# Optimization experiments

Hardware: AMD Instinct MI355X
Metric: run time of the kernel (lower is better)

The kernel has to match this reference:

```python
import jax, jax.numpy as jnp
import numpy as np

N = 100000
E = 3200000
IN_DIM = 256
HID = 64
OUT = 40


def setup_inputs() -> dict:
    key = jax.random.key(0)
    ks = jax.random.split(key, 8)
    x = jax.random.normal(ks[0], (N, IN_DIM), dtype=jnp.float32)
    edge_index = jax.random.randint(ks[1], (2, E), 0, N, dtype=jnp.int64)
    # Glorot-ish init for weights
    W1 = jax.random.normal(ks[2], (IN_DIM, HID), dtype=jnp.float32) / np.sqrt(IN_DIM)
    b1 = jnp.zeros((HID,), dtype=jnp.float32)
    W2 = jax.random.normal(ks[3], (HID, HID), dtype=jnp.float32) / np.sqrt(HID)
    b2 = jnp.zeros((HID,), dtype=jnp.float32)
    W3 = jax.random.normal(ks[4], (HID, OUT), dtype=jnp.float32) / np.sqrt(HID)
    b3 = jax.random.normal(ks[5], (OUT,), dtype=jnp.float32) * 0.01
    return {"x": x, "edge_index": edge_index,
            "W1": W1, "b1": b1, "W2": W2, "b2": b2, "W3": W3, "b3": b3}


def _gcn_norm(edge_index, n):
    # Add self-loops, compute symmetric normalization deg^-1/2 A deg^-1/2
    loop = jnp.arange(n, dtype=edge_index.dtype)
    src = jnp.concatenate([edge_index[0], loop])
    dst = jnp.concatenate([edge_index[1], loop])
    deg = jax.ops.segment_sum(jnp.ones_like(dst, dtype=jnp.float32), dst,
                              num_segments=n)
    dinv = jnp.where(deg > 0, jax.lax.rsqrt(deg), 0.0)
    norm = dinv[src] * dinv[dst]  # [E+N]
    return src, dst, norm


def _gcn_conv(x, src, dst, norm, W, b, n):
    h = x @ W                                  # transform first (small dim)
    msg = h[src] * norm[:, None]               # gather + scale
    out = jax.ops.segment_sum(msg, dst, num_segments=n)  # scatter-add
    return out + b


def reference(x, edge_index, W1, b1, W2, b2, W3, b3):
    n = x.shape[0]
    src, dst, norm = _gcn_norm(edge_index, n)
    h = jax.nn.relu(_gcn_conv(x, src, dst, norm, W1, b1, n))
    h = jax.nn.relu(_gcn_conv(h, src, dst, norm, W2, b2, n))
    logits = h @ W3 + b3
    return jax.nn.log_softmax(logits, axis=1)
```

## Files before the change

kernel.cpp:

```cpp
#include <hip/hip_runtime.h>
#include <hip/hip_fp16.h>
#include <cstdint>


constexpr int CHUNK = 8192;
constexpr int BKCAP = 8192;

__global__ __launch_bounds__(256) void p2_localsort(
        const int* __restrict__ esrc, const int* __restrict__ edst, int E,
        unsigned* __restrict__ pairs1, int* __restrict__ cntMat,
        int* __restrict__ startMat, int NBK) {
    __shared__ int hist[1024];
    __shared__ int wsum[256];
    __shared__ unsigned lp[CHUNK];
    const int t = threadIdx.x, blk = blockIdx.x;
    const int base = blk * CHUNK;
    const int cnt = min(CHUNK, E - base);
    for (int i = t; i < 1024; i += 256) hist[i] = 0;
    __syncthreads();
    for (int i = t; i < cnt; i += 256) atomicAdd(&hist[edst[base + i] >> 7], 1);
    __syncthreads();
    int h0 = hist[4*t], h1 = hist[4*t+1], h2 = hist[4*t+2], h3 = hist[4*t+3];
    int s = h0 + h1 + h2 + h3;
    wsum[t] = s; __syncthreads();
    #pragma unroll
    for (int o = 1; o < 256; o <<= 1) {
        int x = (t >= o) ? wsum[t - o] : 0;
        __syncthreads(); wsum[t] += x; __syncthreads();
    }
    int run = wsum[t] - s;
    int e0 = run, e1 = run + h0, e2 = e1 + h1, e3 = e2 + h2;
    hist[4*t] = e0; hist[4*t+1] = e1; hist[4*t+2] = e2; hist[4*t+3] = e3;
    if (4*t     < NBK) { cntMat[(size_t)blk*NBK + 4*t]     = h0; startMat[(size_t)blk*NBK + 4*t]     = e0; }
    if (4*t + 1 < NBK) { cntMat[(size_t)blk*NBK + 4*t + 1] = h1; startMat[(size_t)blk*NBK + 4*t + 1] = e1; }
    if (4*t + 2 < NBK) { cntMat[(size_t)blk*NBK + 4*t + 2] = h2; startMat[(size_t)blk*NBK + 4*t + 2] = e2; }
    if (4*t + 3 < NBK) { cntMat[(size_t)blk*NBK + 4*t + 3] = h3; startMat[(size_t)blk*NBK + 4*t + 3] = e3; }
    __syncthreads();
    for (int i = t; i < cnt; i += 256) {
        int d = edst[base + i];
        int pos = atomicAdd(&hist[d >> 7], 1);
        lp[pos] = ((unsigned)(d & 127) << 17) | (unsigned)esrc[base + i];
    }
    __syncthreads();
    for (int i = t; i < cnt; i += 256) pairs1[base + i] = lp[i];
}

__global__ __launch_bounds__(256) void p3_colscan(int* __restrict__ cntMat,
        int* __restrict__ TB, int nchunks, int NBK) {
    __shared__ int buf[512];
    const int t = threadIdx.x, b = blockIdx.x;
    int v0 = (t < nchunks) ? cntMat[(size_t)t*NBK + b] : 0;
    int v1 = (t + 256 < nchunks) ? cntMat[(size_t)(t + 256)*NBK + b] : 0;
    buf[t] = v0; buf[t + 256] = v1; __syncthreads();
    #pragma unroll
    for (int o = 1; o < 512; o <<= 1) {
        int x0 = (t >= o) ? buf[t - o] : 0;
        int x1 = (t + 256 >= o) ? buf[t + 256 - o] : 0;
        __syncthreads(); buf[t] += x0; buf[t + 256] += x1; __syncthreads();
    }
    if (t < nchunks) cntMat[(size_t)t*NBK + b] = buf[t] - v0;
    if (t + 256 < nchunks) cntMat[(size_t)(t + 256)*NBK + b] = buf[t + 256] - v1;
    if (t == 0) TB[b] = buf[511];
}

__global__ __launch_bounds__(256) void p4_scan(const int* __restrict__ TB,
        int* __restrict__ bucketBase, int NBK, int E) {
    __shared__ int buf[1024];
    __shared__ int wsum[256];
    const int t = threadIdx.x;
    for (int i = t; i < 1024; i += 256) buf[i] = (i < NBK) ? TB[i] : 0;
    __syncthreads();
    int h0 = buf[4*t], h1 = buf[4*t+1], h2 = buf[4*t+2], h3 = buf[4*t+3];
    int s = h0 + h1 + h2 + h3;
    wsum[t] = s; __syncthreads();
    #pragma unroll
    for (int o = 1; o < 256; o <<= 1) {
        int x = (t >= o) ? wsum[t - o] : 0;
        __syncthreads(); wsum[t] += x; __syncthreads();
    }
    int run = wsum[t] - s;
    int e0 = run, e1 = run + h0, e2 = e1 + h1, e3 = e2 + h2;
    if (4*t     < NBK) bucketBase[4*t]     = e0;
    if (4*t + 1 < NBK) bucketBase[4*t + 1] = e1;
    if (4*t + 2 < NBK) bucketBase[4*t + 2] = e2;
    if (4*t + 3 < NBK) bucketBase[4*t + 3] = e3;
    if (t == 0) bucketBase[NBK] = E;
}

__global__ __launch_bounds__(256) void p6_sortcsr(
        const unsigned* __restrict__ pairs1, const int* __restrict__ cumMat,
        const int* __restrict__ startMat, const int* __restrict__ TB,
        const int* __restrict__ bucketBase, int nchunks, int NBK,
        int* __restrict__ csrc, int* __restrict__ rofs,
        float* __restrict__ dinv, int N, int E) {
    __shared__ unsigned lp[BKCAP];
    __shared__ int ccum[512];
    __shared__ int cstart[512];
    __shared__ int hist[128];
    __shared__ int sc[128];
    __shared__ int foffs[128];
    const int t = threadIdx.x, b = blockIdx.x;
    const int total0 = TB[b];
    const int total = min(total0, BKCAP);
    const int base = bucketBase[b];
    for (int i = t; i < nchunks; i += 256) {
        ccum[i]   = cumMat[(size_t)i * NBK + b];
        cstart[i] = startMat[(size_t)i * NBK + b];
    }
    if (t < 128) hist[t] = 0;
    if (t == 0) ccum[nchunks] = total0;
    __syncthreads();
    for (int i = t; i < total; i += 256) {
        int lo = 0, hi = nchunks - 1;
        while (lo < hi) {
            int mid = (lo + hi + 1) >> 1;
            if (ccum[mid] <= i) lo = mid; else hi = mid - 1;
        }
        unsigned v = pairs1[(size_t)lo * CHUNK + cstart[lo] + (i - ccum[lo])];
        lp[i] = v;
        atomicAdd(&hist[v >> 17], 1);
    }
    __syncthreads();
    if (t < 128) sc[t] = hist[t];
    __syncthreads();
    #pragma unroll
    for (int o = 1; o < 128; o <<= 1) {
        int x = (t >= o && t < 128) ? sc[t - o] : 0;
        __syncthreads();
        if (t < 128) sc[t] += x;
        __syncthreads();
    }
    if (t < 128) {
        int excl = sc[t] - hist[t];
        foffs[t] = excl;
        int node = b * 128 + t;
        if (node < N) {
            rofs[node] = base + excl;
            dinv[node] = rsqrtf((float)hist[t] + 1.0f);
        }
    }
    if (b == 0 && t == 255) rofs[N] = E;
    __syncthreads();
    for (int i = t; i < total; i += 256) {
        unsigned v = lp[i];
        int pos = atomicAdd(&foffs[v >> 17], 1);
        csrc[base + pos] = (int)(v & 0x1FFFFu);
    }
}

template<int K>
__global__ __launch_bounds__(256) void k_gemm(const float* __restrict__ X,
        const float* __restrict__ Wm, const float* __restrict__ dinv,
        __half* __restrict__ G, int nrows) {
    constexpr int BK = 32;
    constexpr int NCH = K / BK;
    constexpr int XP = 68;
    __shared__ float Xs[BK * XP];
    __shared__ float Ws[BK * 64];
    const int t = threadIdx.x;
    const int cg = t & 15;
    const int rg = t >> 4;
    const int brow = blockIdx.x * 64;

    float acc[4][4];
    #pragma unroll
    for (int r = 0; r < 4; ++r)
        #pragma unroll
        for (int c = 0; c < 4; ++c) acc[r][c] = 0.f;

    for (int ch = 0; ch < NCH; ++ch) {
        if (ch) __syncthreads();
        #pragma unroll
        for (int i = 0; i < 2; ++i) {
            int f = t + i * 256;
            int r = f >> 3, c4 = f & 7;
            int gr = brow + r;
            float4 v = make_float4(0.f, 0.f, 0.f, 0.f);
            if (gr < nrows)
                v = *(const float4*)(X + (size_t)gr * K + ch * BK + c4 * 4);
            int rsw = r ^ (c4 << 2);
            Xs[(c4 * 4 + 0) * XP + rsw] = v.x;
            Xs[(c4 * 4 + 1) * XP + rsw] = v.y;
            Xs[(c4 * 4 + 2) * XP + rsw] = v.z;
            Xs[(c4 * 4 + 3) * XP + rsw] = v.w;
        }
        #pragma unroll
        for (int i = 0; i < 2; ++i) {
            int f = t + i * 256;
            int k = f >> 4, c4 = f & 15;
            *(float4*)(Ws + k * 64 + c4 * 4) =
                *(const float4*)(Wm + (size_t)(ch * BK + k) * 64 + c4 * 4);
        }
        __syncthreads();

        #pragma unroll
        for (int k = 0; k < BK; ++k) {
            const int xsw = (k >> 2) << 2;
            float4 xa = *(const float4*)(Xs + k * XP + ((rg * 4) ^ xsw));
            float4 wv = *(const float4*)(Ws + k * 64 + cg * 4);
            acc[0][0] += xa.x * wv.x; acc[0][1] += xa.x * wv.y;
            acc[0][2] += xa.x * wv.z; acc[0][3] += xa.x * wv.w;
            acc[1][0] += xa.y * wv.x; acc[1][1] += xa.y * wv.y;
            acc[1][2] += xa.y * wv.z; acc[1][3] += xa.y * wv.w;
            acc[2][0] += xa.z * wv.x; acc[2][1] += xa.z * wv.y;
            acc[2][2] += xa.z * wv.z; acc[2][3] += xa.z * wv.w;
            acc[3][0] += xa.w * wv.x; acc[3][1] += xa.w * wv.y;
            acc[3][2] += xa.w * wv.z; acc[3][3] += xa.w * wv.w;
        }
    }
    #pragma unroll
    for (int r = 0; r < 4; ++r) {
        int gr = brow + rg * 4 + r;
        if (gr < nrows) {
            float dv = dinv[gr];
            __half2 h01 = __floats2half2_rn(acc[r][0] * dv, acc[r][1] * dv);
            __half2 h23 = __floats2half2_rn(acc[r][2] * dv, acc[r][3] * dv);
            uint2 pk;
            pk.x = *(unsigned*)&h01; pk.y = *(unsigned*)&h23;
            *(uint2*)(G + (size_t)gr * 64 + cg * 4) = pk;
        }
    }
}

#define ACC8(A0, A1, V) { \
    float2 f0_ = __half22float2(*(const __half2*)&(V).x); \
    float2 f1_ = __half22float2(*(const __half2*)&(V).y); \
    float2 f2_ = __half22float2(*(const __half2*)&(V).z); \
    float2 f3_ = __half22float2(*(const __half2*)&(V).w); \
    (A0).x += f0_.x; (A0).y += f0_.y; (A0).z += f1_.x; (A0).w += f1_.y; \
    (A1).x += f2_.x; (A1).y += f2_.y; (A1).z += f3_.x; (A1).w += f3_.y; }

__global__ __launch_bounds__(256) void k_agg(const __half* __restrict__ G,
        const int* __restrict__ rofs, const int* __restrict__ csrc,
        const float* __restrict__ dinv, const float* __restrict__ bias,
        float* __restrict__ H, int nrows) {
    const int l = threadIdx.x & 63;
    const int g = l >> 3;
    const int p = l & 7;
    const int d = blockIdx.x * 4 + (threadIdx.x >> 6);
    if (d >= nrows) return;
    const int beg = rofs[d], end = rofs[d + 1];
    float4 a0 = make_float4(0.f, 0.f, 0.f, 0.f);
    float4 a1 = make_float4(0.f, 0.f, 0.f, 0.f);

    int e = beg + g;
    for (; e + 8 < end; e += 16) {
        int s0 = csrc[e];
        int s1 = csrc[e + 8];
        uint4 v0 = *(const uint4*)(G + (size_t)s0 * 64 + p * 8);
        uint4 v1 = *(const uint4*)(G + (size_t)s1 * 64 + p * 8);
        ACC8(a0, a1, v0)
        ACC8(a0, a1, v1)
    }
    if (e < end) {
        int s = csrc[e];
        uint4 v = *(const uint4*)(G + (size_t)s * 64 + p * 8);
        ACC8(a0, a1, v)
    }
    #pragma unroll
    for (int off = 8; off <= 32; off <<= 1) {
        a0.x += __shfl_xor(a0.x, off); a0.y += __shfl_xor(a0.y, off);
        a0.z += __shfl_xor(a0.z, off); a0.w += __shfl_xor(a0.w, off);
        a1.x += __shfl_xor(a1.x, off); a1.y += __shfl_xor(a1.y, off);
        a1.z += __shfl_xor(a1.z, off); a1.w += __shfl_xor(a1.w, off);
    }
    if (g == 0) {
        uint4 sv = *(const uint4*)(G + (size_t)d * 64 + p * 8);
        float2 s0 = __half22float2(*(const __half2*)&sv.x);
        float2 s1 = __half22float2(*(const __half2*)&sv.y);
        float2 s2 = __half22float2(*(const __half2*)&sv.z);
        float2 s3 = __half22float2(*(const __half2*)&sv.w);
        const float dv = dinv[d];
        const float4* B4 = (const float4*)bias;
        float4 b0 = B4[p * 2], b1 = B4[p * 2 + 1];
        float4 o0, o1;
        o0.x = fmaxf((a0.x + s0.x) * dv + b0.x, 0.f);
        o0.y = fmaxf((a0.y + s0.y) * dv + b0.y, 0.f);
        o0.z = fmaxf((a0.z + s1.x) * dv + b0.z, 0.f);
        o0.w = fmaxf((a0.w + s1.y) * dv + b0.w, 0.f);
        o1.x = fmaxf((a1.x + s2.x) * dv + b1.x, 0.f);
        o1.y = fmaxf((a1.y + s2.y) * dv + b1.y, 0.f);
        o1.z = fmaxf((a1.z + s3.x) * dv + b1.z, 0.f);
        o1.w = fmaxf((a1.w + s3.y) * dv + b1.w, 0.f);
        float4* H4 = (float4*)(H + (size_t)d * 64 + p * 8);
        H4[0] = o0; H4[1] = o1;
    }
}

__global__ __launch_bounds__(256) void k_final(const float* __restrict__ H,
        const float* __restrict__ W3, const float* __restrict__ b3,
        float* __restrict__ out, int nrows) {
    constexpr int HP = 68;
    constexpr int OP = 44;
    __shared__ float wl[64 * 40];
    __shared__ float bl[40];
    __shared__ float Hs[256 * HP];
    const int t = threadIdx.x;
    for (int i = t; i < 640; i += 256)
        ((float4*)wl)[i] = ((const float4*)W3)[i];
    if (t < 40) bl[t] = b3[t];
    const int brow = blockIdx.x * 256;
    const int rows = min(256, nrows - brow);
    for (int i = t; i < rows * 16; i += 256) {
        int r = i >> 4, c = i & 15;
        float4 v = ((const float4*)(H + (size_t)(brow + r) * 64))[c];
        *(float4*)&Hs[r * HP + c * 4] = v;
    }
    __syncthreads();

    float acc[40];
    float lse = 0.f;
    if (t < rows) {
        #pragma unroll
        for (int j = 0; j < 40; ++j) acc[j] = bl[j];
        #pragma unroll
        for (int k4 = 0; k4 < 16; ++k4) {
            float4 h4 = *(const float4*)&Hs[t * HP + k4 * 4];
            float hv[4] = {h4.x, h4.y, h4.z, h4.w};
            #pragma unroll
            for (int c = 0; c < 4; ++c) {
                const float4* wr = (const float4*)(wl + (k4 * 4 + c) * 40);
                #pragma unroll
                for (int j4 = 0; j4 < 10; ++j4) {
                    float4 wv = wr[j4];
                    acc[j4 * 4 + 0] += hv[c] * wv.x;
                    acc[j4 * 4 + 1] += hv[c] * wv.y;
                    acc[j4 * 4 + 2] += hv[c] * wv.z;
                    acc[j4 * 4 + 3] += hv[c] * wv.w;
                }
            }
        }
        float m = acc[0];
        #pragma unroll
        for (int j = 1; j < 40; ++j) m = fmaxf(m, acc[j]);
        float s = 0.f;
        #pragma unroll
        for (int j = 0; j < 40; ++j) s += expf(acc[j] - m);
        lse = m + logf(s);
    }
    __syncthreads();
    float* Os = Hs;
    if (t < rows) {
        #pragma unroll
        for (int j4 = 0; j4 < 10; ++j4)
            *(float4*)&Os[t * OP + j4 * 4] =
                make_float4(acc[j4 * 4 + 0] - lse, acc[j4 * 4 + 1] - lse,
                            acc[j4 * 4 + 2] - lse, acc[j4 * 4 + 3] - lse);
    }
    __syncthreads();
    for (int i = t; i < rows * 40; i += 256) {
        int r = i / 40, c = i - r * 40;
        out[(size_t)brow * 40 + i] = Os[r * OP + c];
    }
}

extern "C" void kernel_launch(void* const* d_in, const int* in_sizes, int n_in,
                              void* d_out, int out_size, void* d_ws, size_t ws_size,
                              hipStream_t stream) {
    const float* x  = (const float*)d_in[0];
    const int*   ei = (const int*)d_in[1];
    const float* W1 = (const float*)d_in[2];
    const float* b1 = (const float*)d_in[3];
    const float* W2 = (const float*)d_in[4];
    const float* b2 = (const float*)d_in[5];
    const float* W3 = (const float*)d_in[6];
    const float* b3 = (const float*)d_in[7];
    float* out = (float*)d_out;

    const int HID = in_sizes[3];
    const int IND = in_sizes[2] / HID;
    const int N   = in_sizes[0] / IND;
    const int E   = in_sizes[1] / 2;
    (void)HID; (void)n_in; (void)out_size; (void)ws_size;

    const int NBK     = (N + 127) >> 7;
    const int nchunks = (E + CHUNK - 1) / CHUNK;

    char* ws = (char*)d_ws;
    size_t off = 0;
    auto alloc = [&](size_t bytes) -> char* {
        char* p = ws + off;
        off = (off + bytes + 255) & ~(size_t)255;
        return p;
    };
    size_t gbytes = (size_t)N * 64 * 2;
    size_t p1bytes = (size_t)E * 4;
    int*      cntMat     = (int*)     alloc((size_t)nchunks * NBK * 4);
    int*      startMat   = (int*)     alloc((size_t)nchunks * NBK * 4);
    int*      TB         = (int*)     alloc((size_t)NBK * 4);
    int*      bucketBase = (int*)     alloc(((size_t)NBK + 1) * 4);
    float*    dinv       = (float*)   alloc((size_t)N * 4);
    int*      rofs       = (int*)     alloc(((size_t)N + 1) * 4);
    int*      csrc       = (int*)     alloc((size_t)E * 4);
    __half*   g          = (__half*)  alloc(gbytes > p1bytes ? gbytes : p1bytes);
    float*    h          = (float*)   alloc((size_t)N * 64 * 4);
    unsigned* pairs1     = (unsigned*)g;

    const int* esrc = ei;
    const int* edst = ei + E;
    const int gM = (N + 63) / 64;
    const int gN = (N + 255) / 256;

    p2_localsort<<<nchunks, 256, 0, stream>>>(esrc, edst, E, pairs1, cntMat, startMat, NBK);
    p3_colscan  <<<NBK, 256, 0, stream>>>(cntMat, TB, nchunks, NBK);
    p4_scan     <<<1, 256, 0, stream>>>(TB, bucketBase, NBK, E);
    p6_sortcsr  <<<NBK, 256, 0, stream>>>(pairs1, cntMat, startMat, TB, bucketBase,
                                          nchunks, NBK, csrc, rofs, dinv, N, E);

    k_gemm<256> <<<gM, 256, 0, stream>>>(x, W1, dinv, g, N);
    k_agg       <<<(N + 3) / 4, 256, 0, stream>>>(g, rofs, csrc, dinv, b1, h, N);
    k_gemm<64>  <<<gM, 256, 0, stream>>>(h, W2, dinv, g, N);
    k_agg       <<<(N + 3) / 4, 256, 0, stream>>>(g, rofs, csrc, dinv, b2, h, N);
    k_final     <<<gN, 256, 0, stream>>>(h, W3, b3, out, N);
}
```

Measured before the change: 289.5 us.

## Use bf16 MFMA for feature GEMMs and half-precision accumulation in aggregation

Replaces the fp32 SIMT register-tiled GEMM with a persistent-wave kernel that converts X and W to bf16 and uses 16x16x32 MFMA instructions, with W staged transposed in LDS. Separately, the neighbour aggregation now accumulates in packed fp16 (hadd2) and reduces via shuffles of packed halves instead of fp32. This aims to cut GEMM ALU time and aggregation instruction count, at the cost of reduced precision (bf16 inputs, fp16 accumulation over ~33 neighbours) and scalar 2-byte output stores. The tiling also assumes nrows is a multiple of 16, which holds for N=100000.

```diff
diff --git a/kernel.cpp b/kernel.cpp
--- a/kernel.cpp
+++ b/kernel.cpp
@@ -5,6 +5,15 @@
 
 constexpr int CHUNK = 8192;
 constexpr int BKCAP = 8192;
+
+typedef __attribute__((ext_vector_type(8))) short bf16x8;
+typedef __attribute__((ext_vector_type(4))) float f32x4;
+
+__device__ __forceinline__ int cvt2bf(float a, float b) {
+    int r;
+    asm volatile("v_cvt_pk_bf16_f32 %0, %1, %2" : "=v"(r) : "v"(a), "v"(b));
+    return r;
+}
 
 __global__ __launch_bounds__(256) void p2_localsort(
         const int* __restrict__ esrc, const int* __restrict__ edst, int E,
@@ -152,83 +161,55 @@
 __global__ __launch_bounds__(256) void k_gemm(const float* __restrict__ X,
         const float* __restrict__ Wm, const float* __restrict__ dinv,
         __half* __restrict__ G, int nrows) {
-    constexpr int BK = 32;
-    constexpr int NCH = K / BK;
-    constexpr int XP = 68;
-    __shared__ float Xs[BK * XP];
-    __shared__ float Ws[BK * 64];
+    constexpr int KP = K + 8;
+    __shared__ unsigned short Wt[64 * KP];
     const int t = threadIdx.x;
-    const int cg = t & 15;
-    const int rg = t >> 4;
-    const int brow = blockIdx.x * 64;
-
-    float acc[4][4];
-    #pragma unroll
-    for (int r = 0; r < 4; ++r)
-        #pragma unroll
-        for (int c = 0; c < 4; ++c) acc[r][c] = 0.f;
-
-    for (int ch = 0; ch < NCH; ++ch) {
-        if (ch) __syncthreads();
-        #pragma unroll
-        for (int i = 0; i < 2; ++i) {
-            int f = t + i * 256;
-            int r = f >> 3, c4 = f & 7;
-            int gr = brow + r;
-            float4 v = make_float4(0.f, 0.f, 0.f, 0.f);
-            if (gr < nrows)
-                v = *(const float4*)(X + (size_t)gr * K + ch * BK + c4 * 4);
-            int rsw = r ^ (c4 << 2);
-            Xs[(c4 * 4 + 0) * XP + rsw] = v.x;
-            Xs[(c4 * 4 + 1) * XP + rsw] = v.y;
-            Xs[(c4 * 4 + 2) * XP + rsw] = v.z;
-            Xs[(c4 * 4 + 3) * XP + rsw] = v.w;
-        }
-        #pragma unroll
-        for (int i = 0; i < 2; ++i) {
-            int f = t + i * 256;
-            int k = f >> 4, c4 = f & 15;
-            *(float4*)(Ws + k * 64 + c4 * 4) =
-                *(const float4*)(Wm + (size_t)(ch * BK + k) * 64 + c4 * 4);
-        }
-        __syncthreads();
-
-        #pragma unroll
-        for (int k = 0; k < BK; ++k) {
-            const int xsw = (k >> 2) << 2;
-            float4 xa = *(const float4*)(Xs + k * XP + ((rg * 4) ^ xsw));
-            float4 wv = *(const float4*)(Ws + k * 64 + cg * 4);
-            acc[0][0] += xa.x * wv.x; acc[0][1] += xa.x * wv.y;
-            acc[0][2] += xa.x * wv.z; acc[0][3] += xa.x * wv.w;
-            acc[1][0] += xa.y * wv.x; acc[1][1] += xa.y * wv.y;
-            acc[1][2] += xa.y * wv.z; acc[1][3] += xa.y * wv.w;
-            acc[2][0] += xa.z * wv.x; acc[2][1] += xa.z * wv.y;
-            acc[2][2] += xa.z * wv.z; acc[2][3] += xa.z * wv.w;
-            acc[3][0] += xa.w * wv.x; acc[3][1] += xa.w * wv.y;
-            acc[3][2] += xa.w * wv.z; acc[3][3] += xa.w * wv.w;
-        }
-    }
-    #pragma unroll
-    for (int r = 0; r < 4; ++r) {
-        int gr = brow + rg * 4 + r;
-        if (gr < nrows) {
-            float dv = dinv[gr];
-            __half2 h01 = __floats2half2_rn(acc[r][0] * dv, acc[r][1] * dv);
-            __half2 h23 = __floats2half2_rn(acc[r][2] * dv, acc[r][3] * dv);
-            uint2 pk;
-            pk.x = *(unsigned*)&h01; pk.y = *(unsigned*)&h23;
-            *(uint2*)(G + (size_t)gr * 64 + cg * 4) = pk;
-        }
-    }
-}
-
-#define ACC8(A0, A1, V) { \
-    float2 f0_ = __half22float2(*(const __half2*)&(V).x); \
-    float2 f1_ = __half22float2(*(const __half2*)&(V).y); \
-    float2 f2_ = __half22float2(*(const __half2*)&(V).z); \
-    float2 f3_ = __half22float2(*(const __half2*)&(V).w); \
-    (A0).x += f0_.x; (A0).y += f0_.y; (A0).z += f1_.x; (A0).w += f1_.y; \
-    (A1).x += f2_.x; (A1).y += f2_.y; (A1).z += f3_.x; (A1).w += f3_.y; }
+    for (int i = t; i < K * 64; i += 256) {
+        int k = i >> 6, n = i & 63;
+        Wt[n * KP + k] = (unsigned short)(cvt2bf(Wm[i], Wm[i]) & 0xFFFF);
+    }
+    __syncthreads();
+    const int l  = t & 63;
+    const int c16 = l & 15;
+    const int g4  = l >> 4;
+    const int wglob  = blockIdx.x * 4 + (t >> 6);
+    const int nwaves = gridDim.x * 4;
+    const int ntiles = nrows >> 4;
+
+    for (int tile = wglob; tile < ntiles; tile += nwaves) {
+        const int rbase = tile * 16;
+        f32x4 acc[4] = {{0,0,0,0},{0,0,0,0},{0,0,0,0},{0,0,0,0}};
+        const float* xrow = X + (size_t)(rbase + c16) * K + g4 * 8;
+        #pragma unroll
+        for (int kc = 0; kc < K / 32; ++kc) {
+            float4 u = *(const float4*)(xrow + kc * 32);
+            float4 v = *(const float4*)(xrow + kc * 32 + 4);
+            int4 ap;
+            ap.x = cvt2bf(u.x, u.y); ap.y = cvt2bf(u.z, u.w);
+            ap.z = cvt2bf(v.x, v.y); ap.w = cvt2bf(v.z, v.w);
+            bf16x8 a = *(bf16x8*)&ap;
+            #pragma unroll
+            for (int cg = 0; cg < 4; ++cg) {
+                bf16x8 bb = *(bf16x8*)(&Wt[(cg * 16 + c16) * KP + kc * 32 + g4 * 8]);
+                acc[cg] = __builtin_amdgcn_mfma_f32_16x16x32_bf16(a, bb, acc[cg], 0, 0, 0);
+            }
+        }
+        #pragma unroll
+        for (int r = 0; r < 4; ++r) {
+            int grow = rbase + g4 * 4 + r;
+            float dv = dinv[grow];
+            #pragma unroll
+            for (int cg = 0; cg < 4; ++cg)
+                G[(size_t)grow * 64 + cg * 16 + c16] = __float2half(acc[cg][r] * dv);
+        }
+    }
+}
+
+#define ACC8H(HA, V) { \
+    HA[0] = __hadd2(HA[0], *(const __half2*)&(V).x); \
+    HA[1] = __hadd2(HA[1], *(const __half2*)&(V).y); \
+    HA[2] = __hadd2(HA[2], *(const __half2*)&(V).z); \
+    HA[3] = __hadd2(HA[3], *(const __half2*)&(V).w); }
 
 __global__ __launch_bounds__(256) void k_agg(const __half* __restrict__ G,
         const int* __restrict__ rofs, const int* __restrict__ csrc,
@@ -240,8 +221,9 @@
     const int d = blockIdx.x * 4 + (threadIdx.x >> 6);
     if (d >= nrows) return;
     const int beg = rofs[d], end = rofs[d + 1];
-    float4 a0 = make_float4(0.f, 0.f, 0.f, 0.f);
-    float4 a1 = make_float4(0.f, 0.f, 0.f, 0.f);
+    __half2 ha[4];
+    #pragma unroll
+    for (int q = 0; q < 4; ++q) ha[q] = __half2(__float2half(0.f), __float2half(0.f));
 
     int e = beg + g;
     for (; e + 8 < end; e += 16) {
@@ -249,22 +231,25 @@
         int s1 = csrc[e + 8];
         uint4 v0 = *(const uint4*)(G + (size_t)s0 * 64 + p * 8);
         uint4 v1 = *(const uint4*)(G + (size_t)s1 * 64 + p * 8);
-        ACC8(a0, a1, v0)
-        ACC8(a0, a1, v1)
+        ACC8H(ha, v0)
+        ACC8H(ha, v1)
     }
     if (e < end) {
         int s = csrc[e];
         uint4 v = *(const uint4*)(G + (size_t)s * 64 + p * 8);
-        ACC8(a0, a1, v)
+        ACC8H(ha, v)
     }
     #pragma unroll
     for (int off = 8; off <= 32; off <<= 1) {
-        a0.x += __shfl_xor(a0.x, off); a0.y += __shfl_xor(a0.y, off);
-        a0.z += __shfl_xor(a0.z, off); a0.w += __shfl_xor(a0.w, off);
-        a1.x += __shfl_xor(a1.x, off); a1.y += __shfl_xor(a1.y, off);
-        a1.z += __shfl_xor(a1.z, off); a1.w += __shfl_xor(a1.w, off);
+        #pragma unroll
+        for (int q = 0; q < 4; ++q) {
+            int o = __shfl_xor(*(int*)&ha[q], off);
+            ha[q] = __hadd2(ha[q], *(__half2*)&o);
+        }
     }
     if (g == 0) {
+        float2 a0 = __half22float2(ha[0]), a1 = __half22float2(ha[1]);
+        float2 a2 = __half22float2(ha[2]), a3 = __half22float2(ha[3]);
         uint4 sv = *(const uint4*)(G + (size_t)d * 64 + p * 8);
         float2 s0 = __half22float2(*(const __half2*)&sv.x);
         float2 s1 = __half22float2(*(const __half2*)&sv.y);
@@ -276,12 +261,12 @@
         float4 o0, o1;
         o0.x = fmaxf((a0.x + s0.x) * dv + b0.x, 0.f);
         o0.y = fmaxf((a0.y + s0.y) * dv + b0.y, 0.f);
-        o0.z = fmaxf((a0.z + s1.x) * dv + b0.z, 0.f);
-        o0.w = fmaxf((a0.w + s1.y) * dv + b0.w, 0.f);
-        o1.x = fmaxf((a1.x + s2.x) * dv + b1.x, 0.f);
-        o1.y = fmaxf((a1.y + s2.y) * dv + b1.y, 0.f);
-        o1.z = fmaxf((a1.z + s3.x) * dv + b1.z, 0.f);
-        o1.w = fmaxf((a1.w + s3.y) * dv + b1.w, 0.f);
+        o0.z = fmaxf((a1.x + s1.x) * dv + b0.z, 0.f);
+        o0.w = fmaxf((a1.y + s1.y) * dv + b0.w, 0.f);
+        o1.x = fmaxf((a2.x + s2.x) * dv + b1.x, 0.f);
+        o1.y = fmaxf((a2.y + s2.y) * dv + b1.y, 0.f);
+        o1.z = fmaxf((a3.x + s3.x) * dv + b1.z, 0.f);
+        o1.w = fmaxf((a3.y + s3.y) * dv + b1.w, 0.f);
         float4* H4 = (float4*)(H + (size_t)d * 64 + p * 8);
         H4[0] = o0; H4[1] = o1;
     }
@@ -398,7 +383,7 @@
 
     const int* esrc = ei;
     const int* edst = ei + E;
-    const int gM = (N + 63) / 64;
+    const int gG = 782;
     const int gN = (N + 255) / 256;
 
     p2_localsort<<<nchunks, 256, 0, stream>>>(esrc, edst, E, pairs1, cntMat, startMat, NBK);
@@ -407,9 +392,9 @@
     p6_sortcsr  <<<NBK, 256, 0, stream>>>(pairs1, cntMat, startMat, TB, bucketBase,
                                           nchunks, NBK, csrc, rofs, dinv, N, E);
 
-    k_gemm<256> <<<gM, 256, 0, stream>>>(x, W1, dinv, g, N);
+    k_gemm<256> <<<gG, 256, 0, stream>>>(x, W1, dinv, g, N);
     k_agg       <<<(N + 3) / 4, 256, 0, stream>>>(g, rofs, csrc, dinv, b1, h, N);
-    k_gemm<64>  <<<gM, 256, 0, stream>>>(h, W2, dinv, g, N);
+    k_gemm<64>  <<<gG, 256, 0, stream>>>(h, W2, dinv, g, N);
     k_agg       <<<(N + 3) / 4, 256, 0, stream>>>(g, rofs, csrc, dinv, b2, h, N);
     k_final     <<<gN, 256, 0, stream>>>(h, W3, b3, out, N);
 }
```

New measurement: 270.2 us. -6.7%, faster.

## Fuse W2 GEMM into first aggregation and final projection into second

Applied to the files above, without the earlier changes.

The second-layer GEMM moves into the first aggregation kernel and the W3 projection plus log-softmax into the second, using wavefront shuffles over the per-node hidden vector. This removes the fp32 H round trip and two kernel launches. Gather accumulation also switches from fp32 to packed half2 adds, which cuts ALU work but can lose precision on high-degree nodes. Each aggregation block now loads the weight matrix into shared memory and runs a 64-step shuffle-FMA loop per node, which is extra per-block overhead.

```diff
diff --git a/kernel.cpp b/kernel.cpp
--- a/kernel.cpp
+++ b/kernel.cpp
@@ -222,136 +222,145 @@
     }
 }
 
-#define ACC8(A0, A1, V) { \
-    float2 f0_ = __half22float2(*(const __half2*)&(V).x); \
-    float2 f1_ = __half22float2(*(const __half2*)&(V).y); \
-    float2 f2_ = __half22float2(*(const __half2*)&(V).z); \
-    float2 f3_ = __half22float2(*(const __half2*)&(V).w); \
-    (A0).x += f0_.x; (A0).y += f0_.y; (A0).z += f1_.x; (A0).w += f1_.y; \
-    (A1).x += f2_.x; (A1).y += f2_.y; (A1).z += f3_.x; (A1).w += f3_.y; }
-
-__global__ __launch_bounds__(256) void k_agg(const __half* __restrict__ G,
+#define ACC8H(HA, V) { \
+    HA[0] = __hadd2(HA[0], *(const __half2*)&(V).x); \
+    HA[1] = __hadd2(HA[1], *(const __half2*)&(V).y); \
+    HA[2] = __hadd2(HA[2], *(const __half2*)&(V).z); \
+    HA[3] = __hadd2(HA[3], *(const __half2*)&(V).w); }
+
+#define GATHER_REDUCE(G_, beg_, end_, g_, p_, HA) { \
+    int e = (beg_) + (g_); \
+    for (; e + 8 < (end_); e += 16) { \
+        int s0 = csrc[e]; \
+        int s1 = csrc[e + 8]; \
+        uint4 v0 = *(const uint4*)((G_) + (size_t)s0 * 64 + (p_) * 8); \
+        uint4 v1 = *(const uint4*)((G_) + (size_t)s1 * 64 + (p_) * 8); \
+        ACC8H(HA, v0) \
+        ACC8H(HA, v1) \
+    } \
+    if (e < (end_)) { \
+        int s = csrc[e]; \
+        uint4 v = *(const uint4*)((G_) + (size_t)s * 64 + (p_) * 8); \
+        ACC8H(HA, v) \
+    } \
+    _Pragma("unroll") \
+    for (int off = 8; off <= 32; off <<= 1) { \
+        _Pragma("unroll") \
+        for (int q = 0; q < 4; ++q) { \
+            int o = __shfl_xor(*(int*)&HA[q], off); \
+            HA[q] = __hadd2(HA[q], *(__half2*)&o); \
+        } \
+    } }
+
+__global__ __launch_bounds__(256) void k_agg_mid(const __half* __restrict__ G,
         const int* __restrict__ rofs, const int* __restrict__ csrc,
-        const float* __restrict__ dinv, const float* __restrict__ bias,
-        float* __restrict__ H, int nrows) {
-    const int l = threadIdx.x & 63;
+        const float* __restrict__ dinv, const float* __restrict__ b1,
+        const float* __restrict__ W2, __half* __restrict__ G2, int nrows) {
+    __shared__ float W2s[64 * 64];
+    const int t = threadIdx.x;
+    for (int i = t; i < 1024; i += 256)
+        ((float4*)W2s)[i] = ((const float4*)W2)[i];
+    __syncthreads();
+    const int l = t & 63;
     const int g = l >> 3;
     const int p = l & 7;
-    const int d = blockIdx.x * 4 + (threadIdx.x >> 6);
+    const int d = blockIdx.x * 4 + (t >> 6);
     if (d >= nrows) return;
     const int beg = rofs[d], end = rofs[d + 1];
-    float4 a0 = make_float4(0.f, 0.f, 0.f, 0.f);
-    float4 a1 = make_float4(0.f, 0.f, 0.f, 0.f);
-
-    int e = beg + g;
-    for (; e + 8 < end; e += 16) {
-        int s0 = csrc[e];
-        int s1 = csrc[e + 8];
-        uint4 v0 = *(const uint4*)(G + (size_t)s0 * 64 + p * 8);
-        uint4 v1 = *(const uint4*)(G + (size_t)s1 * 64 + p * 8);
-        ACC8(a0, a1, v0)
-        ACC8(a0, a1, v1)
-    }
-    if (e < end) {
-        int s = csrc[e];
-        uint4 v = *(const uint4*)(G + (size_t)s * 64 + p * 8);
-        ACC8(a0, a1, v)
-    }
-    #pragma unroll
-    for (int off = 8; off <= 32; off <<= 1) {
-        a0.x += __shfl_xor(a0.x, off); a0.y += __shfl_xor(a0.y, off);
-        a0.z += __shfl_xor(a0.z, off); a0.w += __shfl_xor(a0.w, off);
-        a1.x += __shfl_xor(a1.x, off); a1.y += __shfl_xor(a1.y, off);
-        a1.z += __shfl_xor(a1.z, off); a1.w += __shfl_xor(a1.w, off);
-    }
-    if (g == 0) {
-        uint4 sv = *(const uint4*)(G + (size_t)d * 64 + p * 8);
-        float2 s0 = __half22float2(*(const __half2*)&sv.x);
-        float2 s1 = __half22float2(*(const __half2*)&sv.y);
-        float2 s2 = __half22float2(*(const __half2*)&sv.z);
-        float2 s3 = __half22float2(*(const __half2*)&sv.w);
-        const float dv = dinv[d];
-        const float4* B4 = (const float4*)bias;
-        float4 b0 = B4[p * 2], b1 = B4[p * 2 + 1];
-        float4 o0, o1;
-        o0.x = fmaxf((a0.x + s0.x) * dv + b0.x, 0.f);
-        o0.y = fmaxf((a0.y + s0.y) * dv + b0.y, 0.f);
-        o0.z = fmaxf((a0.z + s1.x) * dv + b0.z, 0.f);
-        o0.w = fmaxf((a0.w + s1.y) * dv + b0.w, 0.f);
-        o1.x = fmaxf((a1.x + s2.x) * dv + b1.x, 0.f);
-        o1.y = fmaxf((a1.y + s2.y) * dv + b1.y, 0.f);
-        o1.z = fmaxf((a1.z + s3.x) * dv + b1.z, 0.f);
-        o1.w = fmaxf((a1.w + s3.y) * dv + b1.w, 0.f);
-        float4* H4 = (float4*)(H + (size_t)d * 64 + p * 8);
-        H4[0] = o0; H4[1] = o1;
-    }
-}
-
-__global__ __launch_bounds__(256) void k_final(const float* __restrict__ H,
+    __half2 ha[4];
+    #pragma unroll
+    for (int q = 0; q < 4; ++q) ha[q] = __half2(__float2half(0.f), __float2half(0.f));
+    GATHER_REDUCE(G, beg, end, g, p, ha)
+
+    uint4 sv = *(const uint4*)(G + (size_t)d * 64 + p * 8);
+    const float dv = dinv[d];
+    float4 bb0 = *(const float4*)(b1 + p * 8);
+    float4 bb1 = *(const float4*)(b1 + p * 8 + 4);
+    float2 a0 = __half22float2(ha[0]), a1 = __half22float2(ha[1]);
+    float2 a2 = __half22float2(ha[2]), a3 = __half22float2(ha[3]);
+    float2 s0 = __half22float2(*(const __half2*)&sv.x);
+    float2 s1 = __half22float2(*(const __half2*)&sv.y);
+    float2 s2 = __half22float2(*(const __half2*)&sv.z);
+    float2 s3 = __half22float2(*(const __half2*)&sv.w);
+    float h1[8];
+    h1[0] = fmaxf((a0.x + s0.x) * dv + bb0.x, 0.f);
+    h1[1] = fmaxf((a0.y + s0.y) * dv + bb0.y, 0.f);
+    h1[2] = fmaxf((a1.x + s1.x) * dv + bb0.z, 0.f);
+    h1[3] = fmaxf((a1.y + s1.y) * dv + bb0.w, 0.f);
+    h1[4] = fmaxf((a2.x + s2.x) * dv + bb1.x, 0.f);
+    h1[5] = fmaxf((a2.y + s2.y) * dv + bb1.y, 0.f);
+    h1[6] = fmaxf((a3.x + s3.x) * dv + bb1.z, 0.f);
+    h1[7] = fmaxf((a3.y + s3.y) * dv + bb1.w, 0.f);
+
+    float acc = 0.f;
+    #pragma unroll
+    for (int k = 0; k < 64; ++k) {
+        float hk = __shfl(h1[k & 7], k >> 3);
+        acc += hk * W2s[k * 64 + l];
+    }
+    G2[(size_t)d * 64 + l] = __float2half(acc * dv);
+}
+
+__global__ __launch_bounds__(256) void k_agg_out(const __half* __restrict__ G2,
+        const int* __restrict__ rofs, const int* __restrict__ csrc,
+        const float* __restrict__ dinv, const float* __restrict__ b2,
         const float* __restrict__ W3, const float* __restrict__ b3,
         float* __restrict__ out, int nrows) {
-    constexpr int HP = 68;
-    constexpr int OP = 44;
-    __shared__ float wl[64 * 40];
-    __shared__ float bl[40];
-    __shared__ float Hs[256 * HP];
+    __shared__ float W3s[64 * 40 + 64];
+    __shared__ float b3s[64];
     const int t = threadIdx.x;
     for (int i = t; i < 640; i += 256)
-        ((float4*)wl)[i] = ((const float4*)W3)[i];
-    if (t < 40) bl[t] = b3[t];
-    const int brow = blockIdx.x * 256;
-    const int rows = min(256, nrows - brow);
-    for (int i = t; i < rows * 16; i += 256) {
-        int r = i >> 4, c = i & 15;
-        float4 v = ((const float4*)(H + (size_t)(brow + r) * 64))[c];
-        *(float4*)&Hs[r * HP + c * 4] = v;
-    }
-    __syncthreads();
-
-    float acc[40];
-    float lse = 0.f;
-    if (t < rows) {
-        #pragma unroll
-        for (int j = 0; j < 40; ++j) acc[j] = bl[j];
-        #pragma unroll
-        for (int k4 = 0; k4 < 16; ++k4) {
-            float4 h4 = *(const float4*)&Hs[t * HP + k4 * 4];
-            float hv[4] = {h4.x, h4.y, h4.z, h4.w};
-            #pragma unroll
-            for (int c = 0; c < 4; ++c) {
-                const float4* wr = (const float4*)(wl + (k4 * 4 + c) * 40);
-                #pragma unroll
-                for (int j4 = 0; j4 < 10; ++j4) {
-                    float4 wv = wr[j4];
-                    acc[j4 * 4 + 0] += hv[c] * wv.x;
-                    acc[j4 * 4 + 1] += hv[c] * wv.y;
-                    acc[j4 * 4 + 2] += hv[c] * wv.z;
-                    acc[j4 * 4 + 3] += hv[c] * wv.w;
-                }
-            }
-        }
-        float m = acc[0];
-        #pragma unroll
-        for (int j = 1; j < 40; ++j) m = fmaxf(m, acc[j]);
-        float s = 0.f;
-        #pragma unroll
-        for (int j = 0; j < 40; ++j) s += expf(acc[j] - m);
-        lse = m + logf(s);
-    }
-    __syncthreads();
-    float* Os = Hs;
-    if (t < rows) {
-        #pragma unroll
-        for (int j4 = 0; j4 < 10; ++j4)
-            *(float4*)&Os[t * OP + j4 * 4] =
-                make_float4(acc[j4 * 4 + 0] - lse, acc[j4 * 4 + 1] - lse,
-                            acc[j4 * 4 + 2] - lse, acc[j4 * 4 + 3] - lse);
-    }
-    __syncthreads();
-    for (int i = t; i < rows * 40; i += 256) {
-        int r = i / 40, c = i - r * 40;
-        out[(size_t)brow * 40 + i] = Os[r * OP + c];
-    }
+        ((float4*)W3s)[i] = ((const float4*)W3)[i];
+    if (t < 64) b3s[t] = (t < 40) ? b3[t] : 0.f;
+    if (t >= 64 && t < 128) W3s[64 * 40 + (t - 64)] = 0.f;
+    __syncthreads();
+    const int l = t & 63;
+    const int g = l >> 3;
+    const int p = l & 7;
+    const int d = blockIdx.x * 4 + (t >> 6);
+    if (d >= nrows) return;
+    const int beg = rofs[d], end = rofs[d + 1];
+    __half2 ha[4];
+    #pragma unroll
+    for (int q = 0; q < 4; ++q) ha[q] = __half2(__float2half(0.f), __float2half(0.f));
+    GATHER_REDUCE(G2, beg, end, g, p, ha)
+
+    uint4 sv = *(const uint4*)(G2 + (size_t)d * 64 + p * 8);
+    const float dv = dinv[d];
+    float4 bb0 = *(const float4*)(b2 + p * 8);
+    float4 bb1 = *(const float4*)(b2 + p * 8 + 4);
+    float2 a0 = __half22float2(ha[0]), a1 = __half22float2(ha[1]);
+    float2 a2 = __half22float2(ha[2]), a3 = __half22float2(ha[3]);
+    float2 s0 = __half22float2(*(const __half2*)&sv.x);
+    float2 s1 = __half22float2(*(const __half2*)&sv.y);
+    float2 s2 = __half22float2(*(const __half2*)&sv.z);
+    float2 s3 = __half22float2(*(const __half2*)&sv.w);
+    float h2[8];
+    h2[0] = fmaxf((a0.x + s0.x) * dv + bb0.x, 0.f);
+    h2[1] = fmaxf((a0.y + s0.y) * dv + bb0.y, 0.f);
+    h2[2] = fmaxf((a1.x + s1.x) * dv + bb0.z, 0.f);
+    h2[3] = fmaxf((a1.y + s1.y) * dv + bb0.w, 0.f);
+    h2[4] = fmaxf((a2.x + s2.x) * dv + bb1.x, 0.f);
+    h2[5] = fmaxf((a2.y + s2.y) * dv + bb1.y, 0.f);
+    h2[6] = fmaxf((a3.x + s3.x) * dv + bb1.z, 0.f);
+    h2[7] = fmaxf((a3.y + s3.y) * dv + bb1.w, 0.f);
+
+    float acc = b3s[l];
+    #pragma unroll
+    for (int k = 0; k < 64; ++k) {
+        float hk = __shfl(h2[k & 7], k >> 3);
+        acc += hk * W3s[k * 40 + l];
+    }
+    float v = (l < 40) ? acc : -3.4e38f;
+    float m = v;
+    #pragma unroll
+    for (int off = 1; off < 64; off <<= 1) m = fmaxf(m, __shfl_xor(m, off));
+    float ex = (l < 40) ? expf(v - m) : 0.f;
+    float ssum = ex;
+    #pragma unroll
+    for (int off = 1; off < 64; off <<= 1) ssum += __shfl_xor(ssum, off);
+    float lse = m + logf(ssum);
+    if (l < 40) out[(size_t)d * 40 + l] = acc - lse;
 }
 
 extern "C" void kernel_launch(void* const* d_in, const int* in_sizes, int n_in,
@@ -393,13 +402,13 @@
     int*      rofs       = (int*)     alloc(((size_t)N + 1) * 4);
     int*      csrc       = (int*)     alloc((size_t)E * 4);
     __half*   g          = (__half*)  alloc(gbytes > p1bytes ? gbytes : p1bytes);
-    float*    h          = (float*)   alloc((size_t)N * 64 * 4);
+    __half*   g2         = (__half*)  alloc(gbytes);
     unsigned* pairs1     = (unsigned*)g;
 
     const int* esrc = ei;
     const int* edst = ei + E;
     const int gM = (N + 63) / 64;
-    const int gN = (N + 255) / 256;
+    const int gA = (N + 3) / 4;
 
     p2_localsort<<<nchunks, 256, 0, stream>>>(esrc, edst, E, pairs1, cntMat, startMat, NBK);
     p3_colscan  <<<NBK, 256, 0, stream>>>(cntMat, TB, nchunks, NBK);
@@ -408,8 +417,6 @@
                                           nchunks, NBK, csrc, rofs, dinv, N, E);
 
     k_gemm<256> <<<gM, 256, 0, stream>>>(x, W1, dinv, g, N);
-    k_agg       <<<(N + 3) / 4, 256, 0, stream>>>(g, rofs, csrc, dinv, b1, h, N);
-    k_gemm<64>  <<<gM, 256, 0, stream>>>(h, W2, dinv, g, N);
-    k_agg       <<<(N + 3) / 4, 256, 0, stream>>>(g, rofs, csrc, dinv, b2, h, N);
-    k_final     <<<gN, 256, 0, stream>>>(h, W3, b3, out, N);
-}
+    k_agg_mid   <<<gA, 256, 0, stream>>>(g, rofs, csrc, dinv, b1, W2, g2, N);
+    k_agg_out   <<<gA, 256, 0, stream>>>(g2, rofs, csrc, dinv, b2, W3, b3, out, N);
+}
```

Result: slower. 382.8 us (+32.2%).
